# Performance work log

Hardware: AMD Instinct MI355X
Metric: run time of the kernel (lower is better)

## Reference

```python
import jax, jax.numpy as jnp
import numpy as np

N = 100000
NEG_SLOPE = 0.2


def gat_conv(x, edge_index, W, att_src, att_dst, bias, heads, out_ch, concat):
    # x: [N, F_in]; W: [F_in, heads*out_ch]; att_*: [heads, out_ch]; bias per PyG
    h = (x @ W).reshape(N, heads, out_ch)  # [N, H, C]
    # add self loops (PyG default add_self_loops=True)
    loop = jnp.arange(N, dtype=edge_index.dtype)
    src = jnp.concatenate([edge_index[0], loop])  # [E+N]
    dst = jnp.concatenate([edge_index[1], loop])
    a_src = jnp.einsum('nhc,hc->nh', h, att_src)  # [N, H]
    a_dst = jnp.einsum('nhc,hc->nh', h, att_dst)
    e = jax.nn.leaky_relu(a_src[src] + a_dst[dst], NEG_SLOPE)  # [E+N, H]
    # segment softmax over destination nodes (numerically stable)
    m = jax.ops.segment_max(e, dst, num_segments=N)
    e = jnp.exp(e - m[dst])
    denom = jax.ops.segment_sum(e, dst, num_segments=N)
    alpha = e / (denom[dst] + 1e-16)  # [E+N, H]
    # weighted scatter-add aggregation
    out = jax.ops.segment_sum(h[src] * alpha[:, :, None], dst, num_segments=N)  # [N,H,C]
    if concat:
        out = out.reshape(N, heads * out_ch)
    else:
        out = out.mean(axis=1)
    return out + bias


def setup_inputs() -> dict:
    key = jax.random.key(0)
    ks = jax.random.split(key, 10)
    F_in, H1, C1, NCLS = 512, 8, 8, 40
    E = 1600000
    x = jax.random.normal(ks[0], (N, F_in), dtype=jnp.float32)
    edge_index = jax.random.randint(ks[1], (2, E), 0, N, dtype=jnp.int64)
    s1 = 1.0 / np.sqrt(F_in)
    s2 = 1.0 / np.sqrt(H1 * C1)
    return {
        'x': x,
        'edge_index': edge_index,
        'W1': jax.random.normal(ks[2], (F_in, H1 * C1), dtype=jnp.float32) * s1,
        'att_src1': jax.random.normal(ks[3], (H1, C1), dtype=jnp.float32) * 0.1,
        'att_dst1': jax.random.normal(ks[4], (H1, C1), dtype=jnp.float32) * 0.1,
        'b1': jnp.zeros((H1 * C1,), dtype=jnp.float32),
        'W2': jax.random.normal(ks[5], (H1 * C1, NCLS), dtype=jnp.float32) * s2,
        'att_src2': jax.random.normal(ks[6], (1, NCLS), dtype=jnp.float32) * 0.1,
        'att_dst2': jax.random.normal(ks[7], (1, NCLS), dtype=jnp.float32) * 0.1,
        'b2': jnp.zeros((NCLS,), dtype=jnp.float32),
    }


def reference(x, edge_index, W1, att_src1, att_dst1, b1, W2, att_src2, att_dst2, b2):
    # dropout in eval mode -> identity
    h = gat_conv(x, edge_index, W1, att_src1, att_dst1, b1, heads=8, out_ch=8, concat=True)
    h = jax.nn.elu(h)
    NCLS = W2.shape[1]
    out = gat_conv(h, edge_index, W2, att_src2, att_dst2, b2, heads=1, out_ch=NCLS, concat=False)
    return jax.nn.softmax(out, axis=1)
```

## Files before the change

kernel.cpp:

```cpp
#include <hip/hip_runtime.h>
#include <math.h>

#define N_NODES 100000
#define FIN     512
#define H1H     8
#define C1C     8
#define HC1     64
#define NCLS    40
#define NEG_SLOPE 0.2f

#define NPB   256
#define NBUK  391
#define EPB   4096

#define TM 128
#define TN 64
#define BK 16
#define XS_LD 132

__global__ __launch_bounds__(256) void k_gemm1(const float* __restrict__ x,
                                               const float* __restrict__ W1,
                                               const float* __restrict__ att_src,
                                               const float* __restrict__ att_dst,
                                               float* __restrict__ h1,
                                               float* __restrict__ a_src,
                                               float* __restrict__ a_dst) {
    __shared__ float xs[2][BK][XS_LD];
    __shared__ float ws[2][BK][TN];
    const int tx = threadIdx.x;
    const int row_base = blockIdx.x * TM;
    const int cg = (tx & 15) << 2;
    const int rg = (tx >> 4) << 3;

    float4 xr4[2];
    float4 wr4;

    auto load_regs = [&](int k0) {
#pragma unroll
        for (int i = 0; i < 2; i++) {
            const int f  = tx + 256 * i;
            const int r  = f >> 2;
            const int kq = (f & 3) << 2;
            const int gr = row_base + r;
            xr4[i] = (gr < N_NODES) ? *(const float4*)(x + (size_t)gr * FIN + k0 + kq)
                                    : make_float4(0.f, 0.f, 0.f, 0.f);
        }
        {
            const int kk = tx >> 4;
            const int c4 = (tx & 15) << 2;
            wr4 = *(const float4*)(W1 + (size_t)(k0 + kk) * TN + c4);
        }
    };
    auto store_lds = [&](int buf) {
#pragma unroll
        for (int i = 0; i < 2; i++) {
            const int f  = tx + 256 * i;
            const int r  = f >> 2;
            const int kq = (f & 3) << 2;
            xs[buf][kq + 0][r] = xr4[i].x;
            xs[buf][kq + 1][r] = xr4[i].y;
            xs[buf][kq + 2][r] = xr4[i].z;
            xs[buf][kq + 3][r] = xr4[i].w;
        }
        {
            const int kk = tx >> 4;
            const int c4 = (tx & 15) << 2;
            *(float4*)&ws[buf][kk][c4] = wr4;
        }
    };

    float acc[8][4];
#pragma unroll
    for (int i = 0; i < 8; i++)
#pragma unroll
        for (int j = 0; j < 4; j++) acc[i][j] = 0.f;

    load_regs(0);
    store_lds(0);
    __syncthreads();

    int buf = 0;
    for (int k0 = 0; k0 < FIN; k0 += BK, buf ^= 1) {
        const bool more = (k0 + BK < FIN);
        if (more) load_regs(k0 + BK);
#pragma unroll
        for (int k = 0; k < BK; k++) {
            const float4 xa = *(const float4*)&xs[buf][k][rg];
            const float4 xb = *(const float4*)&xs[buf][k][rg + 4];
            const float4 wv = *(const float4*)&ws[buf][k][cg];
            const float xr[8] = {xa.x, xa.y, xa.z, xa.w, xb.x, xb.y, xb.z, xb.w};
#pragma unroll
            for (int i = 0; i < 8; i++) {
                acc[i][0] = fmaf(xr[i], wv.x, acc[i][0]);
                acc[i][1] = fmaf(xr[i], wv.y, acc[i][1]);
                acc[i][2] = fmaf(xr[i], wv.z, acc[i][2]);
                acc[i][3] = fmaf(xr[i], wv.w, acc[i][3]);
            }
        }
        if (more) {
            store_lds(buf ^ 1);
            __syncthreads();
        }
    }

    const float4 asv = *(const float4*)(att_src + cg);
    const float4 adv = *(const float4*)(att_dst + cg);
    const int head = cg >> 3;
#pragma unroll
    for (int i = 0; i < 8; i++) {
        const int gr = row_base + rg + i;
        if (gr < N_NODES)
            *(float4*)(h1 + (size_t)gr * HC1 + cg) =
                make_float4(acc[i][0], acc[i][1], acc[i][2], acc[i][3]);
        float ps = acc[i][0] * asv.x + acc[i][1] * asv.y + acc[i][2] * asv.z + acc[i][3] * asv.w;
        float pd = acc[i][0] * adv.x + acc[i][1] * adv.y + acc[i][2] * adv.z + acc[i][3] * adv.w;
        ps += __shfl_xor(ps, 1, 64);
        pd += __shfl_xor(pd, 1, 64);
        if (!(tx & 1) && gr < N_NODES) {
            a_src[gr * H1H + head] = ps;
            a_dst[gr * H1H + head] = pd;
        }
    }
}

__global__ __launch_bounds__(256) void k_bcnt(const int* __restrict__ dst, int E,
                                              int* __restrict__ gcnt) {
    __shared__ int lcnt[NBUK];
    for (int i = threadIdx.x; i < NBUK; i += 256) lcnt[i] = 0;
    __syncthreads();
    const int e0 = blockIdx.x * EPB;
#pragma unroll
    for (int i = 0; i < EPB / 256; i++) {
        const int e = e0 + i * 256 + threadIdx.x;
        if (e < E) atomicAdd(&lcnt[dst[e] >> 8], 1);
    }
    __syncthreads();
    for (int i = threadIdx.x; i < NBUK; i += 256)
        if (lcnt[i]) atomicAdd(&gcnt[i], lcnt[i]);
}

__global__ __launch_bounds__(512) void k_bscan(const int* __restrict__ gcnt,
                                               int* __restrict__ gbase,
                                               int* __restrict__ gcur, int E) {
    __shared__ int sm[512];
    const int t = threadIdx.x;
    const int v = (t < NBUK) ? gcnt[t] : 0;
    sm[t] = v;
    __syncthreads();
    for (int off = 1; off < 512; off <<= 1) {
        const int u = (t >= off) ? sm[t - off] : 0;
        __syncthreads();
        sm[t] += u;
        __syncthreads();
    }
    if (t < NBUK) {
        const int b = sm[t] - v;
        gbase[t] = b;
        gcur[t]  = b;
    }
    if (t == 0) gbase[NBUK] = E;
}

__global__ __launch_bounds__(256) void k_bfill(const int* __restrict__ src,
                                               const int* __restrict__ dst, int E,
                                               int* __restrict__ gcur,
                                               int2* __restrict__ pairs) {
    __shared__ int lcnt[NBUK];
    __shared__ int lbase[NBUK];
    for (int i = threadIdx.x; i < NBUK; i += 256) lcnt[i] = 0;
    __syncthreads();
    const int e0 = blockIdx.x * EPB;
#pragma unroll
    for (int i = 0; i < EPB / 256; i++) {
        const int e = e0 + i * 256 + threadIdx.x;
        if (e < E) atomicAdd(&lcnt[dst[e] >> 8], 1);
    }
    __syncthreads();
    for (int i = threadIdx.x; i < NBUK; i += 256)
        lbase[i] = lcnt[i] ? atomicAdd(&gcur[i], lcnt[i]) : 0;
    __syncthreads();
#pragma unroll
    for (int i = 0; i < EPB / 256; i++) {
        const int e = e0 + i * 256 + threadIdx.x;
        if (e < E) {
            const int d = dst[e];
            const int pos = atomicAdd(&lbase[d >> 8], 1);
            pairs[pos] = make_int2(src[e], d);
        }
    }
}

__global__ __launch_bounds__(256) void k_bscatter(const int2* __restrict__ pairs,
                                                  const int* __restrict__ gbase,
                                                  int* __restrict__ offs,
                                                  int* __restrict__ srcsort, int E) {
    __shared__ int ldeg[NPB];
    __shared__ int ltmp[NPB];
    __shared__ int lcur[NPB];
    const int b = blockIdx.x;
    const int tx = threadIdx.x;
    const int node0 = b << 8;
    const int pbeg = gbase[b];
    const int cnt  = gbase[b + 1] - pbeg;

    ldeg[tx] = 0;
    __syncthreads();
    for (int i = tx; i < cnt; i += 256)
        atomicAdd(&ldeg[pairs[pbeg + i].y - node0], 1);
    __syncthreads();
    const int v = ldeg[tx];
    ltmp[tx] = v;
    __syncthreads();
    for (int off = 1; off < 256; off <<= 1) {
        const int u = (tx >= off) ? ltmp[tx - off] : 0;
        __syncthreads();
        ltmp[tx] += u;
        __syncthreads();
    }
    const int mypos = pbeg + ltmp[tx] - v;
    if (node0 + tx < N_NODES) offs[node0 + tx] = mypos;
    lcur[tx] = mypos;
    if (b == NBUK - 1 && tx == 0) offs[N_NODES] = E;
    __syncthreads();
    for (int i = tx; i < cnt; i += 256) {
        const int2 p = pairs[pbeg + i];
        const int pos = atomicAdd(&lcur[p.y - node0], 1);
        srcsort[pos] = p.x;
    }
}

__global__ __launch_bounds__(256) void k_agg1(const float* __restrict__ h1,
                                              const float* __restrict__ a_src,
                                              const float* __restrict__ a_dst,
                                              const int* __restrict__ offs,
                                              const int* __restrict__ srcsort,
                                              const float* __restrict__ b1,
                                              float* __restrict__ h1e) {
    const int n = blockIdx.x * 4 + (threadIdx.x >> 6);
    if (n >= N_NODES) return;
    const int lane = threadIdx.x & 63;
    const int hh   = lane >> 3;
    const float adn = a_dst[n * H1H + hh];
    const int beg = offs[n], end = offs[n + 1];

    float e0 = a_src[n * H1H + hh] + adn;
    e0 = e0 > 0.f ? e0 : NEG_SLOPE * e0;
    float m = e0;
    float denom = 1.f;
    float acc = h1[(size_t)n * HC1 + lane];

    int j = beg;
    for (; j + 8 <= end; j += 8) {
        int s[8];
#pragma unroll
        for (int t = 0; t < 8; t++) s[t] = srcsort[j + t];
        float q[8], g[8];
#pragma unroll
        for (int t = 0; t < 8; t++) q[t] = a_src[s[t] * H1H + hh];
#pragma unroll
        for (int t = 0; t < 8; t++) g[t] = h1[(size_t)s[t] * HC1 + lane];
        float f[8];
#pragma unroll
        for (int t = 0; t < 8; t++) {
            const float e = q[t] + adn;
            f[t] = e > 0.f ? e : NEG_SLOPE * e;
        }
        const float cm = fmaxf(fmaxf(fmaxf(f[0], f[1]), fmaxf(f[2], f[3])),
                               fmaxf(fmaxf(f[4], f[5]), fmaxf(f[6], f[7])));
        const float nm = fmaxf(m, cm);
        const float sc = __expf(m - nm);
        float w[8];
#pragma unroll
        for (int t = 0; t < 8; t++) w[t] = __expf(f[t] - nm);
        const float wsum = ((w[0] + w[1]) + (w[2] + w[3])) + ((w[4] + w[5]) + (w[6] + w[7]));
        const float wg = fmaf(w[0], g[0], fmaf(w[1], g[1], fmaf(w[2], g[2], fmaf(w[3], g[3],
                         fmaf(w[4], g[4], fmaf(w[5], g[5], fmaf(w[6], g[6], w[7] * g[7])))))));
        denom = fmaf(denom, sc, wsum);
        acc = fmaf(acc, sc, wg);
        m = nm;
    }
    for (; j + 4 <= end; j += 4) {
        const int s0 = srcsort[j], s1 = srcsort[j + 1];
        const int s2 = srcsort[j + 2], s3 = srcsort[j + 3];
        const float q0 = a_src[s0 * H1H + hh], q1 = a_src[s1 * H1H + hh];
        const float q2 = a_src[s2 * H1H + hh], q3 = a_src[s3 * H1H + hh];
        const float g0 = h1[(size_t)s0 * HC1 + lane];
        const float g1 = h1[(size_t)s1 * HC1 + lane];
        const float g2 = h1[(size_t)s2 * HC1 + lane];
        const float g3 = h1[(size_t)s3 * HC1 + lane];
        float f0 = q0 + adn; f0 = f0 > 0.f ? f0 : NEG_SLOPE * f0;
        float f1 = q1 + adn; f1 = f1 > 0.f ? f1 : NEG_SLOPE * f1;
        float f2 = q2 + adn; f2 = f2 > 0.f ? f2 : NEG_SLOPE * f2;
        float f3 = q3 + adn; f3 = f3 > 0.f ? f3 : NEG_SLOPE * f3;
        const float nm = fmaxf(m, fmaxf(fmaxf(f0, f1), fmaxf(f2, f3)));
        const float sc = __expf(m - nm);
        const float w0 = __expf(f0 - nm), w1 = __expf(f1 - nm);
        const float w2 = __expf(f2 - nm), w3 = __expf(f3 - nm);
        denom = fmaf(denom, sc, (w0 + w1) + (w2 + w3));
        acc = fmaf(acc, sc, fmaf(w0, g0, fmaf(w1, g1, fmaf(w2, g2, w3 * g3))));
        m = nm;
    }
    for (; j < end; j++) {
        const int s = srcsort[j];
        float e = a_src[s * H1H + hh] + adn;
        e = e > 0.f ? e : NEG_SLOPE * e;
        const float g = h1[(size_t)s * HC1 + lane];
        const float nm = fmaxf(m, e);
        const float sc = __expf(m - nm);
        const float w = __expf(e - nm);
        denom = fmaf(denom, sc, w);
        acc = fmaf(acc, sc, w * g);
        m = nm;
    }
    float v = acc / denom + b1[lane];
    h1e[(size_t)n * HC1 + lane] = v > 0.f ? v : (__expf(v) - 1.f);
}

#define TM2 128
__global__ __launch_bounds__(256) void k_gemm2(const float* __restrict__ h1e,
                                               const float* __restrict__ W2,
                                               const float* __restrict__ att_src2,
                                               const float* __restrict__ att_dst2,
                                               float* __restrict__ h2,
                                               float* __restrict__ a_src2,
                                               float* __restrict__ a_dst2) {
    __shared__ float hs[32][65][4];
    __shared__ float w2t[NCLS][68];
    __shared__ float asv[NCLS], adv[NCLS];
    const int tx = threadIdx.x;
    const int node0 = blockIdx.x * TM2;

    for (int f = tx; f < HC1 * NCLS; f += 256) {
        const int k = f / NCLS, c = f - k * NCLS;
        w2t[c][k] = W2[f];
    }
    if (tx < NCLS) {
        asv[tx] = att_src2[tx];
        adv[tx] = att_dst2[tx];
    }
#pragma unroll
    for (int i = 0; i < 8; i++) {
        const int f  = tx + 256 * i;
        const int n  = f >> 4;
        const int k4 = (f & 15) << 2;
        const int gn = node0 + n;
        const float4 v = (gn < N_NODES) ? *(const float4*)(h1e + (size_t)gn * HC1 + k4)
                                        : make_float4(0.f, 0.f, 0.f, 0.f);
        const int ng = n >> 2, ni = n & 3;
        hs[ng][k4 + 0][ni] = v.x;
        hs[ng][k4 + 1][ni] = v.y;
        hs[ng][k4 + 2][ni] = v.z;
        hs[ng][k4 + 3][ni] = v.w;
    }
    __syncthreads();

    const int ng = tx >> 3;
    const int cg = tx & 7;
    const int c0 = cg * 5;

    float acc[4][5];
#pragma unroll
    for (int i = 0; i < 4; i++)
#pragma unroll
        for (int j = 0; j < 5; j++) acc[i][j] = 0.f;

    for (int k = 0; k < HC1; k += 4) {
        float4 hv[4];
#pragma unroll
        for (int t = 0; t < 4; t++) hv[t] = *(const float4*)&hs[ng][k + t][0];
#pragma unroll
        for (int j = 0; j < 5; j++) {
            const float4 wv = *(const float4*)&w2t[c0 + j][k];
            acc[0][j] = fmaf(hv[0].x, wv.x, fmaf(hv[1].x, wv.y, fmaf(hv[2].x, wv.z, fmaf(hv[3].x, wv.w, acc[0][j]))));
            acc[1][j] = fmaf(hv[0].y, wv.x, fmaf(hv[1].y, wv.y, fmaf(hv[2].y, wv.z, fmaf(hv[3].y, wv.w, acc[1][j]))));
            acc[2][j] = fmaf(hv[0].z, wv.x, fmaf(hv[1].z, wv.y, fmaf(hv[2].z, wv.z, fmaf(hv[3].z, wv.w, acc[2][j]))));
            acc[3][j] = fmaf(hv[0].w, wv.x, fmaf(hv[1].w, wv.y, fmaf(hv[2].w, wv.z, fmaf(hv[3].w, wv.w, acc[3][j]))));
        }
    }

    float ps[4], pd[4];
#pragma unroll
    for (int i = 0; i < 4; i++) {
        const int gn = node0 + ng * 4 + i;
        float s = 0.f, d = 0.f;
#pragma unroll
        for (int j = 0; j < 5; j++) {
            s = fmaf(acc[i][j], asv[c0 + j], s);
            d = fmaf(acc[i][j], adv[c0 + j], d);
        }
        ps[i] = s;
        pd[i] = d;
        if (gn < N_NODES) {
#pragma unroll
            for (int j = 0; j < 5; j++)
                h2[(size_t)gn * NCLS + c0 + j] = acc[i][j];
        }
    }
#pragma unroll
    for (int off = 1; off < 8; off <<= 1) {
#pragma unroll
        for (int i = 0; i < 4; i++) {
            ps[i] += __shfl_xor(ps[i], off, 64);
            pd[i] += __shfl_xor(pd[i], off, 64);
        }
    }
    if (cg == 0) {
#pragma unroll
        for (int i = 0; i < 4; i++) {
            const int gn = node0 + ng * 4 + i;
            if (gn < N_NODES) {
                a_src2[gn] = ps[i];
                a_dst2[gn] = pd[i];
            }
        }
    }
}

__global__ __launch_bounds__(256) void k_agg2(const float* __restrict__ h2,
                                              const float* __restrict__ a_src,
                                              const float* __restrict__ a_dst,
                                              const int* __restrict__ offs,
                                              const int* __restrict__ srcsort,
                                              const float* __restrict__ b2,
                                              float* __restrict__ out) {
    const int n = blockIdx.x * 4 + (threadIdx.x >> 6);
    if (n >= N_NODES) return;
    const int lane = threadIdx.x & 63;
    const float adn = a_dst[n];
    const int beg = offs[n], end = offs[n + 1];

    float e0 = a_src[n] + adn;
    e0 = e0 > 0.f ? e0 : NEG_SLOPE * e0;
    float m = e0;
    float denom = 1.f;
    float acc = (lane < NCLS) ? h2[(size_t)n * NCLS + lane] : 0.f;

    int j = beg;
    for (; j + 8 <= end; j += 8) {
        int s[8];
#pragma unroll
        for (int t = 0; t < 8; t++) s[t] = srcsort[j + t];
        float q[8], g[8];
#pragma unroll
        for (int t = 0; t < 8; t++) q[t] = a_src[s[t]];
#pragma unroll
        for (int t = 0; t < 8; t++)
            g[t] = (lane < NCLS) ? h2[(size_t)s[t] * NCLS + lane] : 0.f;
        float f[8];
#pragma unroll
        for (int t = 0; t < 8; t++) {
            const float e = q[t] + adn;
            f[t] = e > 0.f ? e : NEG_SLOPE * e;
        }
        const float cm = fmaxf(fmaxf(fmaxf(f[0], f[1]), fmaxf(f[2], f[3])),
                               fmaxf(fmaxf(f[4], f[5]), fmaxf(f[6], f[7])));
        const float nm = fmaxf(m, cm);
        const float sc = __expf(m - nm);
        float w[8];
#pragma unroll
        for (int t = 0; t < 8; t++) w[t] = __expf(f[t] - nm);
        const float wsum = ((w[0] + w[1]) + (w[2] + w[3])) + ((w[4] + w[5]) + (w[6] + w[7]));
        const float wg = fmaf(w[0], g[0], fmaf(w[1], g[1], fmaf(w[2], g[2], fmaf(w[3], g[3],
                         fmaf(w[4], g[4], fmaf(w[5], g[5], fmaf(w[6], g[6], w[7] * g[7])))))));
        denom = fmaf(denom, sc, wsum);
        acc = fmaf(acc, sc, wg);
        m = nm;
    }
    for (; j + 4 <= end; j += 4) {
        const int s0 = srcsort[j], s1 = srcsort[j + 1];
        const int s2 = srcsort[j + 2], s3 = srcsort[j + 3];
        const float q0 = a_src[s0], q1 = a_src[s1];
        const float q2 = a_src[s2], q3 = a_src[s3];
        float g0 = 0.f, g1 = 0.f, g2 = 0.f, g3 = 0.f;
        if (lane < NCLS) {
            g0 = h2[(size_t)s0 * NCLS + lane];
            g1 = h2[(size_t)s1 * NCLS + lane];
            g2 = h2[(size_t)s2 * NCLS + lane];
            g3 = h2[(size_t)s3 * NCLS + lane];
        }
        float f0 = q0 + adn; f0 = f0 > 0.f ? f0 : NEG_SLOPE * f0;
        float f1 = q1 + adn; f1 = f1 > 0.f ? f1 : NEG_SLOPE * f1;
        float f2 = q2 + adn; f2 = f2 > 0.f ? f2 : NEG_SLOPE * f2;
        float f3 = q3 + adn; f3 = f3 > 0.f ? f3 : NEG_SLOPE * f3;
        const float nm = fmaxf(m, fmaxf(fmaxf(f0, f1), fmaxf(f2, f3)));
        const float sc = __expf(m - nm);
        const float w0 = __expf(f0 - nm), w1 = __expf(f1 - nm);
        const float w2 = __expf(f2 - nm), w3 = __expf(f3 - nm);
        denom = fmaf(denom, sc, (w0 + w1) + (w2 + w3));
        acc = fmaf(acc, sc, fmaf(w0, g0, fmaf(w1, g1, fmaf(w2, g2, w3 * g3))));
        m = nm;
    }
    for (; j < end; j++) {
        const int s = srcsort[j];
        float e = a_src[s] + adn;
        e = e > 0.f ? e : NEG_SLOPE * e;
        const float g = (lane < NCLS) ? h2[(size_t)s * NCLS + lane] : 0.f;
        const float nm = fmaxf(m, e);
        const float sc = __expf(m - nm);
        const float w = __expf(e - nm);
        denom = fmaf(denom, sc, w);
        acc = fmaf(acc, sc, w * g);
        m = nm;
    }
    float o = (lane < NCLS) ? (acc / denom + b2[lane]) : -INFINITY;
    float mx = o;
#pragma unroll
    for (int off = 32; off; off >>= 1) mx = fmaxf(mx, __shfl_xor(mx, off, 64));
    const float ex = (lane < NCLS) ? __expf(o - mx) : 0.f;
    float sm = ex;
#pragma unroll
    for (int off = 32; off; off >>= 1) sm += __shfl_xor(sm, off, 64);
    if (lane < NCLS) out[(size_t)n * NCLS + lane] = ex / sm;
}

extern "C" void kernel_launch(void* const* d_in, const int* in_sizes, int n_in,
                              void* d_out, int out_size, void* d_ws, size_t ws_size,
                              hipStream_t stream) {
    const float* x   = (const float*)d_in[0];
    const int*   ei  = (const int*)d_in[1];
    const float* W1v = (const float*)d_in[2];
    const float* as1 = (const float*)d_in[3];
    const float* ad1 = (const float*)d_in[4];
    const float* b1  = (const float*)d_in[5];
    const float* W2v = (const float*)d_in[6];
    const float* as2 = (const float*)d_in[7];
    const float* ad2 = (const float*)d_in[8];
    const float* b2  = (const float*)d_in[9];
    const int E = in_sizes[1] / 2;
    const int* esrc = ei;
    const int* edst = ei + E;

    char* wp = (char*)d_ws;
    auto alloc = [&](size_t bytes) {
        char* p = wp;
        wp += (bytes + 255) & ~(size_t)255;
        return p;
    };
    float* h1     = (float*)alloc((size_t)N_NODES * HC1 * 4);
    float* h1e    = (float*)alloc((size_t)N_NODES * HC1 * 4);
    float* a_src1 = (float*)alloc((size_t)N_NODES * H1H * 4);
    float* a_dst1 = (float*)alloc((size_t)N_NODES * H1H * 4);
    float* a_src2 = (float*)alloc((size_t)N_NODES * 4);
    float* a_dst2 = (float*)alloc((size_t)N_NODES * 4);
    int*   offs   = (int*)alloc((size_t)(N_NODES + 1) * 4);
    int*   gcnt   = (int*)alloc((size_t)NBUK * 4);
    int*   gbase  = (int*)alloc((size_t)(NBUK + 1) * 4);
    int*   gcur   = (int*)alloc((size_t)NBUK * 4);
    int*   srcsort= (int*)alloc((size_t)E * 4);
    int2*  pairs  = (int2*)alloc((size_t)E * 8);
    float* h2     = h1;

    hipMemsetAsync(gcnt, 0, (size_t)NBUK * 4, stream);

    const int NEB = (E + EPB - 1) / EPB;
    k_gemm1<<<(N_NODES + TM - 1) / TM, 256, 0, stream>>>(x, W1v, as1, ad1, h1, a_src1, a_dst1);
    k_bcnt<<<NEB, 256, 0, stream>>>(edst, E, gcnt);
    k_bscan<<<1, 512, 0, stream>>>(gcnt, gbase, gcur, E);
    k_bfill<<<NEB, 256, 0, stream>>>(esrc, edst, E, gcur, pairs);
    k_bscatter<<<NBUK, 256, 0, stream>>>(pairs, gbase, offs, srcsort, E);
    k_agg1<<<(N_NODES + 3) / 4, 256, 0, stream>>>(h1, a_src1, a_dst1, offs, srcsort, b1, h1e);
    k_gemm2<<<(N_NODES + TM2 - 1) / TM2, 256, 0, stream>>>(h1e, W2v, as2, ad2, h2, a_src2, a_dst2);
    k_agg2<<<(N_NODES + 3) / 4, 256, 0, stream>>>(h2, a_src2, a_dst2, offs, srcsort, b2, (float*)d_out);
}
```

Measured before the change: 587.3 us.

## Replace two-level bucket sort CSR build with global-atomic counting sort

Replaces the bucketed CSR construction (shared-memory bucket counts, pair buffer, per-bucket scatter) with a direct counting sort. Per-node degrees come from global atomics, a three-kernel scan produces offsets, and each edge's source goes straight into place via an atomic cursor per node. This drops the intermediate int2 pairs buffer and one full pass over the edges. In exchange it relies on many contended global atomics to random addresses, and the neighbor order within a node becomes nondeterministic.

```diff
diff --git a/kernel.cpp b/kernel.cpp
--- a/kernel.cpp
+++ b/kernel.cpp
@@ -9,9 +9,8 @@
 #define NCLS    40
 #define NEG_SLOPE 0.2f
 
-#define NPB   256
-#define NBUK  391
-#define EPB   4096
+#define NSBLK 391
+#define GSBLK 2048
 
 #define TM 128
 #define TN 64
@@ -123,28 +122,36 @@
     }
 }
 
-__global__ __launch_bounds__(256) void k_bcnt(const int* __restrict__ dst, int E,
-                                              int* __restrict__ gcnt) {
-    __shared__ int lcnt[NBUK];
-    for (int i = threadIdx.x; i < NBUK; i += 256) lcnt[i] = 0;
+__global__ __launch_bounds__(256) void k_deg(const int* __restrict__ dst, int E,
+                                             int* __restrict__ deg) {
+    for (int e = blockIdx.x * 256 + threadIdx.x; e < E; e += GSBLK * 256)
+        atomicAdd(&deg[dst[e]], 1);
+}
+
+__global__ __launch_bounds__(256) void k_scan1(const int* __restrict__ deg,
+                                               int* __restrict__ offs,
+                                               int* __restrict__ bsum) {
+    __shared__ int sm[256];
+    const int tx = threadIdx.x;
+    const int node = blockIdx.x * 256 + tx;
+    const int v = (node < N_NODES) ? deg[node] : 0;
+    sm[tx] = v;
     __syncthreads();
-    const int e0 = blockIdx.x * EPB;
-#pragma unroll
-    for (int i = 0; i < EPB / 256; i++) {
-        const int e = e0 + i * 256 + threadIdx.x;
-        if (e < E) atomicAdd(&lcnt[dst[e] >> 8], 1);
-    }
-    __syncthreads();
-    for (int i = threadIdx.x; i < NBUK; i += 256)
-        if (lcnt[i]) atomicAdd(&gcnt[i], lcnt[i]);
-}
-
-__global__ __launch_bounds__(512) void k_bscan(const int* __restrict__ gcnt,
-                                               int* __restrict__ gbase,
-                                               int* __restrict__ gcur, int E) {
+    for (int off = 1; off < 256; off <<= 1) {
+        const int u = (tx >= off) ? sm[tx - off] : 0;
+        __syncthreads();
+        sm[tx] += u;
+        __syncthreads();
+    }
+    if (node < N_NODES) offs[node] = sm[tx] - v;
+    if (tx == 255) bsum[blockIdx.x] = sm[255];
+}
+
+__global__ __launch_bounds__(512) void k_scan2(const int* __restrict__ bsum,
+                                               int* __restrict__ bbase) {
     __shared__ int sm[512];
     const int t = threadIdx.x;
-    const int v = (t < NBUK) ? gcnt[t] : 0;
+    const int v = (t < NSBLK) ? bsum[t] : 0;
     sm[t] = v;
     __syncthreads();
     for (int off = 1; off < 512; off <<= 1) {
@@ -153,79 +160,29 @@
         sm[t] += u;
         __syncthreads();
     }
-    if (t < NBUK) {
-        const int b = sm[t] - v;
-        gbase[t] = b;
-        gcur[t]  = b;
-    }
-    if (t == 0) gbase[NBUK] = E;
-}
-
-__global__ __launch_bounds__(256) void k_bfill(const int* __restrict__ src,
-                                               const int* __restrict__ dst, int E,
-                                               int* __restrict__ gcur,
-                                               int2* __restrict__ pairs) {
-    __shared__ int lcnt[NBUK];
-    __shared__ int lbase[NBUK];
-    for (int i = threadIdx.x; i < NBUK; i += 256) lcnt[i] = 0;
-    __syncthreads();
-    const int e0 = blockIdx.x * EPB;
-#pragma unroll
-    for (int i = 0; i < EPB / 256; i++) {
-        const int e = e0 + i * 256 + threadIdx.x;
-        if (e < E) atomicAdd(&lcnt[dst[e] >> 8], 1);
-    }
-    __syncthreads();
-    for (int i = threadIdx.x; i < NBUK; i += 256)
-        lbase[i] = lcnt[i] ? atomicAdd(&gcur[i], lcnt[i]) : 0;
-    __syncthreads();
-#pragma unroll
-    for (int i = 0; i < EPB / 256; i++) {
-        const int e = e0 + i * 256 + threadIdx.x;
-        if (e < E) {
-            const int d = dst[e];
-            const int pos = atomicAdd(&lbase[d >> 8], 1);
-            pairs[pos] = make_int2(src[e], d);
-        }
-    }
-}
-
-__global__ __launch_bounds__(256) void k_bscatter(const int2* __restrict__ pairs,
-                                                  const int* __restrict__ gbase,
-                                                  int* __restrict__ offs,
-                                                  int* __restrict__ srcsort, int E) {
-    __shared__ int ldeg[NPB];
-    __shared__ int ltmp[NPB];
-    __shared__ int lcur[NPB];
-    const int b = blockIdx.x;
-    const int tx = threadIdx.x;
-    const int node0 = b << 8;
-    const int pbeg = gbase[b];
-    const int cnt  = gbase[b + 1] - pbeg;
-
-    ldeg[tx] = 0;
-    __syncthreads();
-    for (int i = tx; i < cnt; i += 256)
-        atomicAdd(&ldeg[pairs[pbeg + i].y - node0], 1);
-    __syncthreads();
-    const int v = ldeg[tx];
-    ltmp[tx] = v;
-    __syncthreads();
-    for (int off = 1; off < 256; off <<= 1) {
-        const int u = (tx >= off) ? ltmp[tx - off] : 0;
-        __syncthreads();
-        ltmp[tx] += u;
-        __syncthreads();
-    }
-    const int mypos = pbeg + ltmp[tx] - v;
-    if (node0 + tx < N_NODES) offs[node0 + tx] = mypos;
-    lcur[tx] = mypos;
-    if (b == NBUK - 1 && tx == 0) offs[N_NODES] = E;
-    __syncthreads();
-    for (int i = tx; i < cnt; i += 256) {
-        const int2 p = pairs[pbeg + i];
-        const int pos = atomicAdd(&lcur[p.y - node0], 1);
-        srcsort[pos] = p.x;
+    if (t < NSBLK) bbase[t] = sm[t] - v;
+}
+
+__global__ __launch_bounds__(256) void k_scan3(const int* __restrict__ bbase,
+                                               int* __restrict__ offs,
+                                               int* __restrict__ cur, int E) {
+    const int node = blockIdx.x * 256 + threadIdx.x;
+    if (node < N_NODES) {
+        const int o = offs[node] + bbase[blockIdx.x];
+        offs[node] = o;
+        cur[node]  = o;
+    }
+    if (node == 0) offs[N_NODES] = E;
+}
+
+__global__ __launch_bounds__(256) void k_fill(const int* __restrict__ src,
+                                              const int* __restrict__ dst, int E,
+                                              int* __restrict__ cur,
+                                              int* __restrict__ srcsort) {
+    for (int e = blockIdx.x * 256 + threadIdx.x; e < E; e += GSBLK * 256) {
+        const int d = dst[e];
+        const int pos = atomicAdd(&cur[d], 1);
+        srcsort[pos] = src[e];
     }
 }
 
@@ -543,21 +500,21 @@
     float* a_src2 = (float*)alloc((size_t)N_NODES * 4);
     float* a_dst2 = (float*)alloc((size_t)N_NODES * 4);
     int*   offs   = (int*)alloc((size_t)(N_NODES + 1) * 4);
-    int*   gcnt   = (int*)alloc((size_t)NBUK * 4);
-    int*   gbase  = (int*)alloc((size_t)(NBUK + 1) * 4);
-    int*   gcur   = (int*)alloc((size_t)NBUK * 4);
+    int*   deg    = (int*)alloc((size_t)N_NODES * 4);
+    int*   cur    = (int*)alloc((size_t)N_NODES * 4);
+    int*   bsum   = (int*)alloc((size_t)NSBLK * 4);
+    int*   bbase  = (int*)alloc((size_t)NSBLK * 4);
     int*   srcsort= (int*)alloc((size_t)E * 4);
-    int2*  pairs  = (int2*)alloc((size_t)E * 8);
     float* h2     = h1;
 
-    hipMemsetAsync(gcnt, 0, (size_t)NBUK * 4, stream);
-
-    const int NEB = (E + EPB - 1) / EPB;
+    hipMemsetAsync(deg, 0, (size_t)N_NODES * 4, stream);
+
     k_gemm1<<<(N_NODES + TM - 1) / TM, 256, 0, stream>>>(x, W1v, as1, ad1, h1, a_src1, a_dst1);
-    k_bcnt<<<NEB, 256, 0, stream>>>(edst, E, gcnt);
-    k_bscan<<<1, 512, 0, stream>>>(gcnt, gbase, gcur, E);
-    k_bfill<<<NEB, 256, 0, stream>>>(esrc, edst, E, gcur, pairs);
-    k_bscatter<<<NBUK, 256, 0, stream>>>(pairs, gbase, offs, srcsort, E);
+    k_deg<<<GSBLK, 256, 0, stream>>>(edst, E, deg);
+    k_scan1<<<NSBLK, 256, 0, stream>>>(deg, offs, bsum);
+    k_scan2<<<1, 512, 0, stream>>>(bsum, bbase);
+    k_scan3<<<NSBLK, 256, 0, stream>>>(bbase, offs, cur, E);
+    k_fill<<<GSBLK, 256, 0, stream>>>(esrc, edst, E, cur, srcsort);
     k_agg1<<<(N_NODES + 3) / 4, 256, 0, stream>>>(h1, a_src1, a_dst1, offs, srcsort, b1, h1e);
     k_gemm2<<<(N_NODES + TM2 - 1) / TM2, 256, 0, stream>>>(h1e, W2v, as2, ad2, h2, a_src2, a_dst2);
     k_agg2<<<(N_NODES + 3) / 4, 256, 0, stream>>>(h2, a_src2, a_dst2, offs, srcsort, b2, (float*)d_out);
```

New measurement: 704.7 us. +20.0%, slower.

## Restructure first GEMM to per-lane rows with wave-uniform W1 scalar loads

Applied to the files above, without the earlier changes.

Rewrites the x@W1 kernel so each block handles 64 rows, each wave owns 16 output columns, and each lane owns one row. W1 is no longer staged in LDS; it is read with wave-uniform addresses (readfirstlane on the wave id) that can become scalar loads, and x is staged in a smaller LDS tile. The goal is to cut LDS traffic and staging work, since each lane now does 16 FMAs per LDS read, while doubling the number of blocks. The trade-offs are less register-level reuse of x per thread, repeated global and scalar reads of W1 per k step, and possible LDS bank conflicts on the transposed stores with the new padding.

```diff
diff --git a/kernel.cpp b/kernel.cpp
--- a/kernel.cpp
+++ b/kernel.cpp
@@ -13,10 +13,9 @@
 #define NBUK  391
 #define EPB   4096
 
-#define TM 128
-#define TN 64
+#define TM 64
 #define BK 16
-#define XS_LD 132
+#define XPAD 68
 
 __global__ __launch_bounds__(256) void k_gemm1(const float* __restrict__ x,
                                                const float* __restrict__ W1,
@@ -25,55 +24,35 @@
                                                float* __restrict__ h1,
                                                float* __restrict__ a_src,
                                                float* __restrict__ a_dst) {
-    __shared__ float xs[2][BK][XS_LD];
-    __shared__ float ws[2][BK][TN];
-    const int tx = threadIdx.x;
+    __shared__ float xs[2][BK][XPAD];
+    const int tx   = threadIdx.x;
+    const int lane = tx & 63;
+    const int wid  = __builtin_amdgcn_readfirstlane(tx >> 6);
+    const int c0   = wid << 4;
     const int row_base = blockIdx.x * TM;
-    const int cg = (tx & 15) << 2;
-    const int rg = (tx >> 4) << 3;
-
-    float4 xr4[2];
-    float4 wr4;
-
+    const int gr   = row_base + lane;
+    const bool valid = gr < N_NODES;
+
+    const int sr  = tx >> 2;
+    const int sk  = (tx & 3) << 2;
+    const int sgr = row_base + sr;
+    const bool svalid = sgr < N_NODES;
+
+    float4 xr4;
     auto load_regs = [&](int k0) {
-#pragma unroll
-        for (int i = 0; i < 2; i++) {
-            const int f  = tx + 256 * i;
-            const int r  = f >> 2;
-            const int kq = (f & 3) << 2;
-            const int gr = row_base + r;
-            xr4[i] = (gr < N_NODES) ? *(const float4*)(x + (size_t)gr * FIN + k0 + kq)
-                                    : make_float4(0.f, 0.f, 0.f, 0.f);
-        }
-        {
-            const int kk = tx >> 4;
-            const int c4 = (tx & 15) << 2;
-            wr4 = *(const float4*)(W1 + (size_t)(k0 + kk) * TN + c4);
-        }
+        xr4 = svalid ? *(const float4*)(x + (size_t)sgr * FIN + k0 + sk)
+                     : make_float4(0.f, 0.f, 0.f, 0.f);
     };
     auto store_lds = [&](int buf) {
-#pragma unroll
-        for (int i = 0; i < 2; i++) {
-            const int f  = tx + 256 * i;
-            const int r  = f >> 2;
-            const int kq = (f & 3) << 2;
-            xs[buf][kq + 0][r] = xr4[i].x;
-            xs[buf][kq + 1][r] = xr4[i].y;
-            xs[buf][kq + 2][r] = xr4[i].z;
-            xs[buf][kq + 3][r] = xr4[i].w;
-        }
-        {
-            const int kk = tx >> 4;
-            const int c4 = (tx & 15) << 2;
-            *(float4*)&ws[buf][kk][c4] = wr4;
-        }
+        xs[buf][sk + 0][sr] = xr4.x;
+        xs[buf][sk + 1][sr] = xr4.y;
+        xs[buf][sk + 2][sr] = xr4.z;
+        xs[buf][sk + 3][sr] = xr4.w;
     };
 
-    float acc[8][4];
-#pragma unroll
-    for (int i = 0; i < 8; i++)
-#pragma unroll
-        for (int j = 0; j < 4; j++) acc[i][j] = 0.f;
+    float acc[16];
+#pragma unroll
+    for (int j = 0; j < 16; j++) acc[j] = 0.f;
 
     load_regs(0);
     store_lds(0);
@@ -85,17 +64,11 @@
         if (more) load_regs(k0 + BK);
 #pragma unroll
         for (int k = 0; k < BK; k++) {
-            const float4 xa = *(const float4*)&xs[buf][k][rg];
-            const float4 xb = *(const float4*)&xs[buf][k][rg + 4];
-            const float4 wv = *(const float4*)&ws[buf][k][cg];
-            const float xr[8] = {xa.x, xa.y, xa.z, xa.w, xb.x, xb.y, xb.z, xb.w};
-#pragma unroll
-            for (int i = 0; i < 8; i++) {
-                acc[i][0] = fmaf(xr[i], wv.x, acc[i][0]);
-                acc[i][1] = fmaf(xr[i], wv.y, acc[i][1]);
-                acc[i][2] = fmaf(xr[i], wv.z, acc[i][2]);
-                acc[i][3] = fmaf(xr[i], wv.w, acc[i][3]);
-            }
+            const float xv = xs[buf][k][lane];
+            const float* wr = W1 + (size_t)(k0 + k) * HC1 + c0;
+#pragma unroll
+            for (int j = 0; j < 16; j++)
+                acc[j] = fmaf(xv, wr[j], acc[j]);
         }
         if (more) {
             store_lds(buf ^ 1);
@@ -103,23 +76,24 @@
         }
     }
 
-    const float4 asv = *(const float4*)(att_src + cg);
-    const float4 adv = *(const float4*)(att_dst + cg);
-    const int head = cg >> 3;
-#pragma unroll
-    for (int i = 0; i < 8; i++) {
-        const int gr = row_base + rg + i;
-        if (gr < N_NODES)
-            *(float4*)(h1 + (size_t)gr * HC1 + cg) =
-                make_float4(acc[i][0], acc[i][1], acc[i][2], acc[i][3]);
-        float ps = acc[i][0] * asv.x + acc[i][1] * asv.y + acc[i][2] * asv.z + acc[i][3] * asv.w;
-        float pd = acc[i][0] * adv.x + acc[i][1] * adv.y + acc[i][2] * adv.z + acc[i][3] * adv.w;
-        ps += __shfl_xor(ps, 1, 64);
-        pd += __shfl_xor(pd, 1, 64);
-        if (!(tx & 1) && gr < N_NODES) {
-            a_src[gr * H1H + head] = ps;
-            a_dst[gr * H1H + head] = pd;
-        }
+    float s0 = 0.f, s1 = 0.f, d0 = 0.f, d1 = 0.f;
+#pragma unroll
+    for (int j = 0; j < 8; j++) {
+        s0 = fmaf(acc[j],     att_src[c0 + j],     s0);
+        d0 = fmaf(acc[j],     att_dst[c0 + j],     d0);
+        s1 = fmaf(acc[8 + j], att_src[c0 + 8 + j], s1);
+        d1 = fmaf(acc[8 + j], att_dst[c0 + 8 + j], d1);
+    }
+    if (valid) {
+#pragma unroll
+        for (int t = 0; t < 4; t++)
+            *(float4*)(h1 + (size_t)gr * HC1 + c0 + 4 * t) =
+                make_float4(acc[4 * t], acc[4 * t + 1], acc[4 * t + 2], acc[4 * t + 3]);
+        const int h0 = wid * 2;
+        a_src[gr * H1H + h0]     = s0;
+        a_src[gr * H1H + h0 + 1] = s1;
+        a_dst[gr * H1H + h0]     = d0;
+        a_dst[gr * H1H + h0 + 1] = d1;
     }
 }
 
```

Result: slower. 661.2 us (+12.6%).
